# Performance work log

Hardware: AMD Instinct MI355X
Metric: run time of the kernel (lower is better)

## Reference

```python
import jax, jax.numpy as jnp
import numpy as np

DIM = 1024
HEADS = 16
HEAD_DIM = DIM // HEADS
MLP = 4 * DIM
EPS = 1e-5


def layer_norm(x, g, b):
    mu = jnp.mean(x, axis=-1, keepdims=True)
    var = jnp.var(x, axis=-1, keepdims=True)
    return (x - mu) * jax.lax.rsqrt(var + EPS) * g + b


def rope_cos_sin(n, d):
    inv_freq = 1.0 / (10000.0 ** (jnp.arange(0, d, 2, dtype=jnp.float32) / d))
    t = jnp.arange(n, dtype=jnp.float32)
    freqs = jnp.outer(t, inv_freq)          # [N, d/2]
    emb = jnp.concatenate([freqs, freqs], -1)  # [N, d]
    return jnp.cos(emb), jnp.sin(emb)


def rotate_half(x):
    x1, x2 = x[..., ::2], x[..., 1::2]
    return jnp.concatenate([-x2, x1], axis=-1)


def setup_inputs() -> dict:
    key = jax.random.key(0)
    ks = jax.random.split(key, 16)
    B, N = 2, 2048
    s = lambda fan_in: 1.0 / np.sqrt(fan_in)
    inp = {
        "x": jax.random.normal(ks[0], (B, N, DIM), jnp.float32),
        "t_emb": jax.random.normal(ks[1], (B, DIM), jnp.float32),
        "norm1_g": jnp.ones((DIM,), jnp.float32),
        "norm1_b": jnp.zeros((DIM,), jnp.float32),
        "Wq": jax.random.normal(ks[2], (DIM, DIM), jnp.float32) * s(DIM),
        "Wk": jax.random.normal(ks[3], (DIM, DIM), jnp.float32) * s(DIM),
        "Wv": jax.random.normal(ks[4], (DIM, DIM), jnp.float32) * s(DIM),
        "Wo": jax.random.normal(ks[5], (DIM, DIM), jnp.float32) * s(DIM),
        "norm2_g": jnp.ones((DIM,), jnp.float32),
        "norm2_b": jnp.zeros((DIM,), jnp.float32),
        "W1": jax.random.normal(ks[6], (DIM, MLP), jnp.float32) * s(DIM),
        "W2": jax.random.normal(ks[7], (MLP, DIM), jnp.float32) * s(MLP),
        "ada_W": jax.random.normal(ks[8], (DIM, 6 * DIM), jnp.float32) * s(DIM),
        "ada_b": jnp.zeros((6 * DIM,), jnp.float32),
    }
    return inp


def reference(x, t_emb, norm1_g, norm1_b, Wq, Wk, Wv, Wo,
              norm2_g, norm2_b, W1, W2, ada_W, ada_b):
    B, N, C = x.shape
    H, D = HEADS, HEAD_DIM
    scale = D ** -0.5

    mod = jax.nn.silu(t_emb) @ ada_W + ada_b          # [B, 6C]
    (shift_msa, scale_msa, gate_msa,
     shift_mlp, scale_mlp, gate_mlp) = jnp.split(mod, 6, axis=-1)

    xn = layer_norm(x, norm1_g, norm1_b) * (1 + scale_msa[:, None, :]) + shift_msa[:, None, :]

    q = (xn @ Wq).reshape(B, N, H, D).transpose(0, 2, 1, 3)  # [B,H,N,D]
    k = (xn @ Wk).reshape(B, N, H, D).transpose(0, 2, 1, 3)
    v = (xn @ Wv).reshape(B, N, H, D).transpose(0, 2, 1, 3)

    cos, sin = rope_cos_sin(N, D)                     # [N, D]
    q = q * cos + rotate_half(q) * sin
    k = k * cos + rotate_half(k) * sin

    attn = jnp.einsum('bhnd,bhmd->bhnm', q, k) * scale  # explicit O(N^2) scores
    attn = jax.nn.softmax(attn, axis=-1)
    out = jnp.einsum('bhnm,bhmd->bhnd', attn, v)

    out = out.transpose(0, 2, 1, 3).reshape(B, N, C) @ Wo
    x = x + gate_msa[:, None, :] * out

    xn = layer_norm(x, norm2_g, norm2_b) * (1 + scale_mlp[:, None, :]) + shift_mlp[:, None, :]
    mlp = jax.nn.gelu(xn @ W1, approximate=False) @ W2
    x = x + gate_mlp[:, None, :] * mlp
    return x
```

## Files before the change

### kernel.cpp

```cpp
#include <hip/hip_runtime.h>
#include <math.h>

#define BB    2
#define NN    2048
#define CDIM  1024
#define HEADS 16
#define HDIM  64
#define MLPD  4096
#define MODC  6144
#define EPSV  1e-5f
#define LOG2E 1.4426950408889634f
#define MSPLIT 16

typedef __attribute__((ext_vector_type(8))) short s8v;
typedef __attribute__((ext_vector_type(4))) float f4v;

__device__ inline unsigned short f2bf(float f) {
  union { float f; unsigned u; } v; v.f = f;
  unsigned r = v.u + 0x7FFFu + ((v.u >> 16) & 1u);
  return (unsigned short)(r >> 16);
}
__device__ inline float bf2f(unsigned short h) {
  union { unsigned u; float f; } v; v.u = ((unsigned)h) << 16;
  return v.f;
}

template<int CTRL>
__device__ __forceinline__ float dpp_max_step(float v) {
  int iv = __float_as_int(v);
  int sh = __builtin_amdgcn_update_dpp(iv, iv, CTRL, 0xF, 0xF, false);
  return fmaxf(v, __int_as_float(sh));
}
__device__ __forceinline__ float max16(float v) {
  v = dpp_max_step<0xB1>(v);
  v = dpp_max_step<0x4E>(v);
  v = dpp_max_step<0x124>(v);
  v = dpp_max_step<0x128>(v);
  return v;
}

__global__ __launch_bounds__(256) void mod_part(
    const float* __restrict__ t_emb, const float* __restrict__ ada_W,
    float* __restrict__ part) {
  int j = blockIdx.x * 256 + threadIdx.x;
  int b = blockIdx.y, ks = blockIdx.z;
  __shared__ float st[64];
  if (threadIdx.x < 64) {
    float v = t_emb[b * CDIM + ks * 64 + threadIdx.x];
    st[threadIdx.x] = v / (1.0f + expf(-v));
  }
  __syncthreads();
  float acc = 0.f;
  const float* wp = ada_W + (size_t)(ks * 64) * MODC + j;
  #pragma unroll 8
  for (int i = 0; i < 64; ++i) acc += st[i] * wp[(size_t)i * MODC];
  part[((size_t)ks * BB + b) * MODC + j] = acc;
}

__global__ __launch_bounds__(256) void mod_reduce(
    const float* __restrict__ part, const float* __restrict__ ada_b,
    float* __restrict__ mod) {
  int idx = blockIdx.x * 256 + threadIdx.x;
  int b = idx / MODC, j = idx % MODC;
  float a = ada_b[j];
  #pragma unroll
  for (int s = 0; s < MSPLIT; ++s) a += part[((size_t)s * BB + b) * MODC + j];
  mod[(size_t)b * MODC + j] = a;
}

__device__ inline float wave_sum64(float v) {
  for (int o = 32; o > 0; o >>= 1) v += __shfl_down(v, o, 64);
  return v;
}

__global__ __launch_bounds__(256) void ln_mod_bf16(
    const float* __restrict__ x, const float* __restrict__ g,
    const float* __restrict__ bta, const float* __restrict__ mod,
    int shift_off, int scale_off, unsigned short* __restrict__ out) {
  int r = blockIdx.x;
  int b = r / NN;
  int t = threadIdx.x;
  const float* xr = x + (size_t)r * CDIM;
  float4 xv = ((const float4*)xr)[t];
  float s  = xv.x + xv.y + xv.z + xv.w;
  float s2 = xv.x*xv.x + xv.y*xv.y + xv.z*xv.z + xv.w*xv.w;
  __shared__ float ws1[4], ws2[4];
  float sw = wave_sum64(s), s2w = wave_sum64(s2);
  int lane = t & 63, wid = t >> 6;
  if (lane == 0) { ws1[wid] = sw; ws2[wid] = s2w; }
  __syncthreads();
  float mu  = (ws1[0] + ws1[1] + ws1[2] + ws1[3]) * (1.0f / CDIM);
  float var = (ws2[0] + ws2[1] + ws2[2] + ws2[3]) * (1.0f / CDIM) - mu * mu;
  float rstd = rsqrtf(var + EPSV);
  const float* mods = mod + (size_t)b * MODC;
  float4 gv = ((const float4*)g)[t];
  float4 bv = ((const float4*)bta)[t];
  float4 sc = ((const float4*)(mods + scale_off))[t];
  float4 sh = ((const float4*)(mods + shift_off))[t];
  ushort4 ov;
  ov.x = f2bf(((xv.x - mu) * rstd * gv.x + bv.x) * (1.0f + sc.x) + sh.x);
  ov.y = f2bf(((xv.y - mu) * rstd * gv.y + bv.y) * (1.0f + sc.y) + sh.y);
  ov.z = f2bf(((xv.z - mu) * rstd * gv.z + bv.z) * (1.0f + sc.z) + sh.z);
  ov.w = f2bf(((xv.w - mu) * rstd * gv.w + bv.w) * (1.0f + sc.w) + sh.w);
  ((ushort4*)(out + (size_t)r * CDIM))[t] = ov;
}

__global__ __launch_bounds__(256) void wcast_all(
    const float* __restrict__ Wq, const float* __restrict__ Wk,
    const float* __restrict__ Wv, const float* __restrict__ Wo,
    const float* __restrict__ W1, const float* __restrict__ W2,
    unsigned short* __restrict__ Wqkvt, unsigned short* __restrict__ Wot,
    unsigned short* __restrict__ W1t, unsigned short* __restrict__ W2t) {
  int bid = blockIdx.x;
  const float* W; unsigned short* Wt; int K, N, t;
  if (bid < 4096) {
    int m = bid >> 10;
    t = bid & 1023;
    K = CDIM; N = CDIM;
    W  = (m == 0) ? Wq : (m == 1) ? Wk : (m == 2) ? Wv : Wo;
    Wt = (m == 3) ? Wot : (Wqkvt + (size_t)m * CDIM * CDIM);
  } else if (bid < 8192) {
    t = bid - 4096; K = CDIM; N = MLPD; W = W1; Wt = W1t;
  } else {
    t = bid - 8192; K = MLPD; N = CDIM; W = W2; Wt = W2t;
  }
  int ntiles = N >> 5;
  int n0 = (t % ntiles) * 32, k0 = (t / ntiles) * 32;
  __shared__ float tile[32][33];
  int tx = threadIdx.x & 31, ty = threadIdx.x >> 5;
  #pragma unroll
  for (int p = 0; p < 4; ++p)
    tile[ty + p * 8][tx] = W[(size_t)(k0 + ty + p * 8) * N + n0 + tx];
  __syncthreads();
  #pragma unroll
  for (int p = 0; p < 4; ++p)
    Wt[(size_t)(n0 + ty + p * 8) * K + k0 + tx] = f2bf(tile[tx][ty + p * 8]);
}

__global__ __launch_bounds__(1024) void mfma_gemm_256(
    const unsigned short* __restrict__ A,
    const unsigned short* __restrict__ Bt,
    int M, int N, int K,
    unsigned short* __restrict__ Ob, unsigned short* __restrict__ Ob2,
    unsigned short* __restrict__ Ob3, int mode) {
  __shared__ unsigned short SH[2 * 32768];
  int tid = threadIdx.x;
  int wave = tid >> 6, lane = tid & 63;
  int quad = lane >> 4, l15 = lane & 15;
  int m0 = blockIdx.y * 256, n0 = blockIdx.x * 256;
  int wr = wave >> 2, wc = wave & 3;

  f4v acc[4][4] = {};

  int srow = lane >> 3;
  int ksrc = ((lane & 7) ^ (lane >> 3)) << 3;
  const int nt = K >> 6;

  #define STAGE_256(T, BUF)                                                    \
    {                                                                          \
      int k0_ = (T) << 6;                                                      \
      unsigned short* ab = SH + (BUF) * 32768 + wave * 1024;                   \
      _Pragma("unroll")                                                        \
      for (int s = 0; s < 2; ++s) {                                            \
        const unsigned short* ga =                                             \
            A + (size_t)(m0 + 16 * wave + 8 * s + srow) * K + k0_ + ksrc;      \
        __builtin_amdgcn_global_load_lds(                                      \
            (const __attribute__((address_space(1))) unsigned int*)(const void*)ga, \
            (__attribute__((address_space(3))) unsigned int*)(void*)(ab + s * 512), \
            16, 0, 0);                                                         \
        const unsigned short* gb =                                             \
            Bt + (size_t)(n0 + 16 * wave + 8 * s + srow) * K + k0_ + ksrc;     \
        __builtin_amdgcn_global_load_lds(                                      \
            (const __attribute__((address_space(1))) unsigned int*)(const void*)gb, \
            (__attribute__((address_space(3))) unsigned int*)(void*)(ab + 16384 + s * 512), \
            16, 0, 0);                                                         \
      }                                                                        \
    }

  STAGE_256(0, 0);
  asm volatile("s_waitcnt vmcnt(0)" ::: "memory");
  __syncthreads();

  int buf = 0;
  for (int t = 0; t < nt; ++t) {
    if (t + 1 < nt) STAGE_256(t + 1, buf ^ 1);

    const unsigned short* Ab = SH + buf * 32768;
    const unsigned short* Bb = Ab + 16384;
    #pragma unroll
    for (int ks = 0; ks < 2; ++ks) {
      int kx = (ks * 32 + quad * 8) ^ ((l15 & 7) << 3);
      s8v af[4], bf[4];
      #pragma unroll
      for (int i = 0; i < 4; ++i)
        af[i] = *(const s8v*)(Ab + (wr * 64 + i * 16 + l15) * 64 + kx);
      #pragma unroll
      for (int j = 0; j < 4; ++j)
        bf[j] = *(const s8v*)(Bb + (wc * 64 + j * 16 + l15) * 64 + kx);
      #pragma unroll
      for (int i = 0; i < 4; ++i)
        #pragma unroll
        for (int j = 0; j < 4; ++j)
          acc[i][j] = __builtin_amdgcn_mfma_f32_16x16x32_bf16(
              af[i], bf[j], acc[i][j], 0, 0, 0);
    }

    if (t + 1 < nt) {
      asm volatile("s_waitcnt vmcnt(0)" ::: "memory");
      __syncthreads();
      buf ^= 1;
    }
  }
  #undef STAGE_256

  #pragma unroll
  for (int i = 0; i < 4; ++i) {
    int rbase = m0 + wr * 64 + i * 16 + quad * 4;
    #pragma unroll
    for (int j = 0; j < 4; ++j) {
      int c = n0 + wc * 64 + j * 16 + l15;
      #pragma unroll
      for (int rg = 0; rg < 4; ++rg) {
        int r = rbase + rg;
        float v = acc[i][j][rg];
        if (mode == 0) {
          unsigned short* dst = (c < 1024) ? Ob : ((c < 2048) ? Ob2 : Ob3);
          dst[(size_t)r * 1024 + (c & 1023)] = f2bf(v);
        } else {
          v = 0.5f * v * (1.0f + erff(v * 0.70710678118f));
          Ob[(size_t)r * N + c] = f2bf(v);
        }
      }
    }
  }
}

__global__ __launch_bounds__(1024) void mfma_gemm_res(
    const unsigned short* __restrict__ A,
    const unsigned short* __restrict__ Bt,
    int M, int N, int K,
    float* __restrict__ O0,
    const float* __restrict__ res, const float* __restrict__ mod,
    int gate_off) {
  __shared__ unsigned short SH[3 * 16384];
  int tid = threadIdx.x;
  int wave = tid >> 6, lane = tid & 63;
  int quad = lane >> 4, l15 = lane & 15;
  int m0 = blockIdx.y * 128, n0 = blockIdx.x * 128;
  int pos = wave & 7;
  int om = pos >> 1, on = pos & 1;
  int ks = wave >> 3;

  f4v acc[2][4] = {};

  int srow = lane >> 3;
  int ksrc = ((lane & 7) ^ (lane >> 3)) << 3;
  const int nt = K >> 6;

  #define STAGE_RES(T, BUF)                                                    \
    {                                                                          \
      int k0_ = (T) << 6;                                                      \
      unsigned short* dsta = SH + (BUF) * 16384 + wave * 512;                  \
      const unsigned short* ga =                                               \
          A + (size_t)(m0 + 8 * wave + srow) * K + k0_ + ksrc;                 \
      __builtin_amdgcn_global_load_lds(                                        \
          (const __attribute__((address_space(1))) unsigned int*)(const void*)ga, \
          (__attribute__((address_space(3))) unsigned int*)(void*)dsta,        \
          16, 0, 0);                                                           \
      const unsigned short* gb =                                               \
          Bt + (size_t)(n0 + 8 * wave + srow) * K + k0_ + ksrc;                \
      __builtin_amdgcn_global_load_lds(                                        \
          (const __attribute__((address_space(1))) unsigned int*)(const void*)gb, \
          (__attribute__((address_space(3))) unsigned int*)(void*)(dsta + 8192), \
          16, 0, 0);                                                           \
    }

  STAGE_RES(0, 0);
  STAGE_RES(1, 1);
  asm volatile("s_waitcnt vmcnt(2)" ::: "memory");
  __syncthreads();

  int kx = (ks * 32 + quad * 8) ^ ((l15 & 7) << 3);

  int rbuf = 0, sbuf = 2;
  for (int t = 0; t < nt; ++t) {
    if (t + 2 < nt) STAGE_RES(t + 2, sbuf);

    const unsigned short* base = SH + rbuf * 16384;
    s8v af[2], bf[4];
    #pragma unroll
    for (int i = 0; i < 2; ++i)
      af[i] = *(const s8v*)(base + (om * 32 + i * 16 + l15) * 64 + kx);
    #pragma unroll
    for (int j = 0; j < 4; ++j)
      bf[j] = *(const s8v*)(base + 8192 + (on * 64 + j * 16 + l15) * 64 + kx);
    #pragma unroll
    for (int i = 0; i < 2; ++i)
      #pragma unroll
      for (int j = 0; j < 4; ++j)
        acc[i][j] = __builtin_amdgcn_mfma_f32_16x16x32_bf16(
            af[i], bf[j], acc[i][j], 0, 0, 0);

    if (t + 2 < nt) {
      asm volatile("s_waitcnt vmcnt(2)" ::: "memory");
    } else if (t + 1 < nt) {
      asm volatile("s_waitcnt vmcnt(0)" ::: "memory");
    }
    __syncthreads();
    rbuf = (rbuf == 2) ? 0 : rbuf + 1;
    sbuf = (sbuf == 2) ? 0 : sbuf + 1;
  }
  #undef STAGE_RES

  float* red = (float*)SH;
  if (wave >= 8) {
    int rb = (wave - 8) * 2304 + lane * 36;
    #pragma unroll
    for (int i = 0; i < 2; ++i)
      #pragma unroll
      for (int j = 0; j < 4; ++j)
        *(f4v*)(red + rb + (i * 4 + j) * 4) = acc[i][j];
  }
  __syncthreads();
  if (wave < 8) {
    int rb = wave * 2304 + lane * 36;
    #pragma unroll
    for (int i = 0; i < 2; ++i)
      #pragma unroll
      for (int j = 0; j < 4; ++j)
        acc[i][j] += *(const f4v*)(red + rb + (i * 4 + j) * 4);
    #pragma unroll
    for (int i = 0; i < 2; ++i) {
      int rbase = m0 + om * 32 + i * 16 + quad * 4;
      #pragma unroll
      for (int j = 0; j < 4; ++j) {
        int c = n0 + on * 64 + j * 16 + l15;
        #pragma unroll
        for (int rg = 0; rg < 4; ++rg) {
          int r = rbase + rg;
          int bb2 = r >> 11;
          O0[(size_t)r * N + c] =
              res[(size_t)r * N + c] + mod[bb2 * MODC + gate_off + c] * acc[i][j][rg];
        }
      }
    }
  }
}

__global__ __launch_bounds__(256) void rope_qk(
    unsigned short* __restrict__ qb, const unsigned short* __restrict__ kb,
    unsigned short* __restrict__ kpack, float qscale) {
  int r = blockIdx.x;
  int b = r / NN, n = r % NN;
  int t = threadIdx.x;
  int isK = blockIdx.y;
  const unsigned short* src = isK ? kb : qb;
  float scale = isK ? 1.0f : qscale;
  __shared__ float row[CDIM];
  __shared__ float csv[32], snv[32];
  if (t < 32) {
    float invf = powf(10000.0f, -(float)t / 32.0f);
    float sn, cs;
    sincosf((float)n * invf, &sn, &cs);
    csv[t] = cs * scale; snv[t] = sn * scale;
  }
  const unsigned short* qr = src + (size_t)r * CDIM;
  ushort4 xv = ((const ushort4*)qr)[t];
  row[t * 4 + 0] = bf2f(xv.x);
  row[t * 4 + 1] = bf2f(xv.y);
  row[t * 4 + 2] = bf2f(xv.z);
  row[t * 4 + 3] = bf2f(xv.w);
  __syncthreads();
  unsigned short o[4];
  int c0 = t * 4;
  #pragma unroll
  for (int q4 = 0; q4 < 4; ++q4) {
    int c = c0 + q4;
    int h = c >> 6, d = c & 63;
    int i = d & 31;
    float rh = (d < 32) ? -row[h * 64 + 2 * d + 1] : row[h * 64 + 2 * (d - 32)];
    o[q4] = f2bf(row[c] * csv[i] + rh * snv[i]);
  }
  if (!isK) {
    ((ushort4*)(qb + (size_t)r * CDIM))[t] = make_ushort4(o[0], o[1], o[2], o[3]);
  } else {
    int h = c0 >> 6, d0 = c0 & 63;
    int half = d0 >> 5, quad = (d0 >> 3) & 3, j0 = d0 & 7;
    int bh = b * HEADS + h;
    int tt = n >> 6, kt = (n >> 4) & 3, l15 = n & 15;
    int lane = quad * 16 + l15;
    size_t off = ((((size_t)bh * 32 + tt) * 8 + kt * 2 + half) * 64 + lane) * 8 + j0;
    unsigned int lo = (unsigned)o[0] | ((unsigned)o[1] << 16);
    unsigned int hi = (unsigned)o[2] | ((unsigned)o[3] << 16);
    *(uint2*)(kpack + off) = make_uint2(lo, hi);
  }
}

__global__ __launch_bounds__(256) void vtrans_pack(
    const unsigned short* __restrict__ vrow, unsigned short* __restrict__ vpack) {
  int t = blockIdx.x;
  int bh = blockIdx.y;
  int b = bh >> 4, h = bh & 15;
  __shared__ unsigned short L[64 * 72];
  int tid = threadIdx.x;
  #pragma unroll
  for (int p = 0; p < 2; ++p) {
    int c = tid + p * 256;
    int key = c >> 3, dc = (c & 7) * 8;
    *(s8v*)(L + key * 72 + dc) =
        *(const s8v*)(vrow + (size_t)(b * NN + t * 64 + key) * CDIM + h * HDIM + dc);
  }
  __syncthreads();
  #pragma unroll
  for (int p = 0; p < 2; ++p) {
    int o = tid + p * 256;
    int f = o >> 6, lane = o & 63;
    int dt = f >> 1, half = f & 1, quad = lane >> 4, l15 = lane & 15;
    int d = dt * 16 + l15;
    unsigned short tmp[8];
    #pragma unroll
    for (int j = 0; j < 8; ++j) {
      int key = (j & 3) * 16 + half * 8 + quad * 2 + (j >> 2);
      tmp[j] = L[key * 72 + d];
    }
    *(s8v*)(vpack + ((((size_t)bh * 32 + t) * 8 + f) * 64 + lane) * 8) = *(s8v*)tmp;
  }
}

__global__ __launch_bounds__(512) void fattn_pack(
    const unsigned short* __restrict__ qb,
    const unsigned short* __restrict__ kpack,
    const unsigned short* __restrict__ vpack,
    unsigned short* __restrict__ ob) {
  int bid = blockIdx.x;
  int qt = bid >> 5, bh = bid & 31;
  int b = bh >> 4, h = bh & 15;
  int tid = threadIdx.x;
  int wave = tid >> 6, lane = tid & 63;
  int quad = lane >> 4, l15 = lane & 15;

  __shared__ unsigned short smem[3 * 8192 + 8 * 2304];
  unsigned short* Pw = smem + 3 * 8192 + wave * 2304;

  int n0 = qt * 256;
  s8v qf[2][2];
  #pragma unroll
  for (int fq = 0; fq < 2; ++fq) {
    int qrow = n0 + wave * 32 + fq * 16 + l15;
    const unsigned short* qp = qb + (size_t)(b * NN + qrow) * CDIM + h * HDIM;
    qf[fq][0] = *(const s8v*)(qp + quad * 8);
    qf[fq][1] = *(const s8v*)(qp + 32 + quad * 8);
  }

  f4v acc[2][4] = {};
  float m_i[2][4], l_i[2][4];
  #pragma unroll
  for (int fq = 0; fq < 2; ++fq)
    #pragma unroll
    for (int r = 0; r < 4; ++r) { m_i[fq][r] = -1e30f; l_i[fq][r] = 0.f; }

  const unsigned short* ksrc = kpack + (size_t)bh * 131072 + wave * 512 + lane * 8;
  const unsigned short* vsrc = vpack + (size_t)bh * 131072 + wave * 512 + lane * 8;

  #define STAGE_ATT(T, BUF)                                                    \
    {                                                                          \
      __builtin_amdgcn_global_load_lds(                                        \
          (const __attribute__((address_space(1))) unsigned int*)(const void*)(ksrc + (size_t)(T) * 4096), \
          (__attribute__((address_space(3))) unsigned int*)(void*)(smem + (BUF) * 8192 + wave * 512), \
          16, 0, 0);                                                           \
      __builtin_amdgcn_global_load_lds(                                        \
          (const __attribute__((address_space(1))) unsigned int*)(const void*)(vsrc + (size_t)(T) * 4096), \
          (__attribute__((address_space(3))) unsigned int*)(void*)(smem + (BUF) * 8192 + 4096 + wave * 512), \
          16, 0, 0);                                                           \
    }

  const int NT = NN / 64;
  STAGE_ATT(0, 0);
  STAGE_ATT(1, 1);
  asm volatile("s_waitcnt vmcnt(2)" ::: "memory");
  __syncthreads();

  int rbuf = 0, sbuf = 2;
  for (int t = 0; t < NT; ++t) {
    if (t + 2 < NT) STAGE_ATT(t + 2, sbuf);

    const unsigned short* kb_ = smem + rbuf * 8192 + lane * 8;
    f4v s4[2][4];
    {
      s8v kf[8];
      #pragma unroll
      for (int f = 0; f < 8; ++f) kf[f] = *(const s8v*)(kb_ + f * 512);
      #pragma unroll
      for (int fq = 0; fq < 2; ++fq)
        #pragma unroll
        for (int kt = 0; kt < 4; ++kt) {
          f4v z = {};
          z = __builtin_amdgcn_mfma_f32_16x16x32_bf16(qf[fq][0], kf[kt * 2], z, 0, 0, 0);
          z = __builtin_amdgcn_mfma_f32_16x16x32_bf16(qf[fq][1], kf[kt * 2 + 1], z, 0, 0, 0);
          s4[fq][kt] = z;
        }
    }

    #pragma unroll
    for (int fq = 0; fq < 2; ++fq)
      #pragma unroll
      for (int r = 0; r < 4; ++r) {
        float mv = fmaxf(fmaxf(s4[fq][0][r], s4[fq][1][r]),
                         fmaxf(s4[fq][2][r], s4[fq][3][r]));
        mv = max16(mv);
        if (!__all(mv - m_i[fq][r] <= 8.0f)) {
          float mnew = fmaxf(m_i[fq][r], mv);
          float alpha = __builtin_amdgcn_exp2f(m_i[fq][r] - mnew);
          m_i[fq][r] = mnew;
          l_i[fq][r] *= alpha;
          acc[fq][0][r] *= alpha; acc[fq][1][r] *= alpha;
          acc[fq][2][r] *= alpha; acc[fq][3][r] *= alpha;
        }
        float ls = 0.f;
        #pragma unroll
        for (int kt = 0; kt < 4; ++kt) {
          float p = __builtin_amdgcn_exp2f(s4[fq][kt][r] - m_i[fq][r]);
          s4[fq][kt][r] = p;
          ls += p;
        }
        l_i[fq][r] += ls;
      }

    #pragma unroll
    for (int fq = 0; fq < 2; ++fq)
      #pragma unroll
      for (int r = 0; r < 4; ++r) {
        unsigned int lo = (__float_as_uint(s4[fq][0][r]) >> 16) |
                          (__float_as_uint(s4[fq][1][r]) & 0xffff0000u);
        unsigned int hi = (__float_as_uint(s4[fq][2][r]) >> 16) |
                          (__float_as_uint(s4[fq][3][r]) & 0xffff0000u);
        *(uint2*)(Pw + (fq * 16 + quad * 4 + r) * 72 + l15 * 4) = make_uint2(lo, hi);
      }

    {
      const unsigned short* vb_ = smem + rbuf * 8192 + 4096 + lane * 8;
      s8v vf[8];
      #pragma unroll
      for (int f = 0; f < 8; ++f) vf[f] = *(const s8v*)(vb_ + f * 512);
      #pragma unroll
      for (int fq = 0; fq < 2; ++fq) {
        s8v pf0 = *(const s8v*)(Pw + (fq * 16 + l15) * 72 + quad * 8);
        s8v pf1 = *(const s8v*)(Pw + (fq * 16 + l15) * 72 + 32 + quad * 8);
        #pragma unroll
        for (int dt = 0; dt < 4; ++dt) {
          acc[fq][dt] = __builtin_amdgcn_mfma_f32_16x16x32_bf16(pf0, vf[dt * 2], acc[fq][dt], 0, 0, 0);
          acc[fq][dt] = __builtin_amdgcn_mfma_f32_16x16x32_bf16(pf1, vf[dt * 2 + 1], acc[fq][dt], 0, 0, 0);
        }
      }
    }

    if (t + 2 < NT) {
      asm volatile("s_waitcnt vmcnt(2)" ::: "memory");
    } else if (t + 1 < NT) {
      asm volatile("s_waitcnt vmcnt(0)" ::: "memory");
    }
    __syncthreads();
    rbuf = (rbuf == 2) ? 0 : rbuf + 1;
    sbuf = (sbuf == 2) ? 0 : sbuf + 1;
  }
  #undef STAGE_ATT

  #pragma unroll
  for (int fq = 0; fq < 2; ++fq)
    #pragma unroll
    for (int r = 0; r < 4; ++r) {
      float l = l_i[fq][r];
      #pragma unroll
      for (int msk = 1; msk < 16; msk <<= 1)
        l += __shfl_xor(l, msk, 64);
      float inv = 1.0f / l;
      size_t row = (size_t)(b * NN + n0 + wave * 32 + fq * 16 + quad * 4 + r);
      unsigned short* op = ob + row * CDIM + h * HDIM;
      #pragma unroll
      for (int dt = 0; dt < 4; ++dt)
        op[dt * 16 + l15] = f2bf(acc[fq][dt][r] * inv);
    }
}

extern "C" void kernel_launch(void* const* d_in, const int* in_sizes, int n_in,
                              void* d_out, int out_size, void* d_ws, size_t ws_size,
                              hipStream_t stream) {
  const float* x    = (const float*)d_in[0];
  const float* temb = (const float*)d_in[1];
  const float* n1g  = (const float*)d_in[2];
  const float* n1b  = (const float*)d_in[3];
  const float* Wq   = (const float*)d_in[4];
  const float* Wk   = (const float*)d_in[5];
  const float* Wv   = (const float*)d_in[6];
  const float* Wo   = (const float*)d_in[7];
  const float* n2g  = (const float*)d_in[8];
  const float* n2b  = (const float*)d_in[9];
  const float* W1   = (const float*)d_in[10];
  const float* W2   = (const float*)d_in[11];
  const float* adaW = (const float*)d_in[12];
  const float* adab = (const float*)d_in[13];
  float* out = (float*)d_out;

  const size_t TOK = (size_t)BB * NN * CDIM;
  float* wsf = (float*)d_ws;
  float* mod     = wsf;
  float* modpart = wsf + 16384;
  unsigned short* tokb  = (unsigned short*)(wsf + 16384 + MSPLIT * BB * MODC);
  unsigned short* qb    = tokb + TOK;
  unsigned short* kb    = qb + TOK;
  unsigned short* kpack = kb + TOK;
  unsigned short* vpack = kpack + TOK;
  unsigned short* Wqkvt = vpack + TOK;
  unsigned short* Wot   = Wqkvt + 3 * CDIM * CDIM;
  unsigned short* W1t   = Wot + CDIM * CDIM;
  unsigned short* W2t   = W1t + CDIM * MLPD;
  unsigned short* h1b   = W2t + MLPD * CDIM;
  unsigned short* vrow  = h1b;
  float* x1 = (float*)qb;

  const int M = BB * NN;

  mod_part<<<dim3(MODC / 256, BB, MSPLIT), 256, 0, stream>>>(temb, adaW, modpart);
  mod_reduce<<<dim3(BB * MODC / 256), 256, 0, stream>>>(modpart, adab, mod);
  ln_mod_bf16<<<dim3(M), 256, 0, stream>>>(x, n1g, n1b, mod, 0, 1024, tokb);

  wcast_all<<<dim3(12288), 256, 0, stream>>>(
      Wq, Wk, Wv, Wo, W1, W2, Wqkvt, Wot, W1t, W2t);

  mfma_gemm_256<<<dim3(3 * CDIM / 256, M / 256), 1024, 0, stream>>>(
      tokb, Wqkvt, M, 3 * CDIM, CDIM, qb, kb, vrow, 0);

  rope_qk<<<dim3(M, 2), 256, 0, stream>>>(qb, kb, kpack, 0.125f * LOG2E);

  vtrans_pack<<<dim3(NN / 64, BB * HEADS), 256, 0, stream>>>(vrow, vpack);

  fattn_pack<<<dim3((NN / 256) * BB * HEADS), 512, 0, stream>>>(
      qb, kpack, vpack, tokb);

  mfma_gemm_res<<<dim3(CDIM / 128, M / 128), 1024, 0, stream>>>(
      tokb, Wot, M, CDIM, CDIM, x1, x, mod, 2048);

  ln_mod_bf16<<<dim3(M), 256, 0, stream>>>(x1, n2g, n2b, mod, 3072, 4096, tokb);

  mfma_gemm_256<<<dim3(MLPD / 256, M / 256), 1024, 0, stream>>>(
      tokb, W1t, M, MLPD, CDIM, h1b, nullptr, nullptr, 1);

  mfma_gemm_res<<<dim3(CDIM / 128, M / 128), 1024, 0, stream>>>(
      h1b, W2t, M, CDIM, MLPD, out, x1, mod, 5120);
}
```

Baseline: 389.1 us.

## Split-K the W2 down-projection GEMM and combine partials with residual

Replaces the final W2 GEMM (K=4096, 256 blocks of 128x128) with a split-K version that launches twice as many blocks, each covering half of K and writing fp32 partial sums into reused workspace buffers. A new elementwise kernel then sums the two partials, applies the gate and adds the residual. This aims to fill more compute units on a GEMM whose grid is small relative to the device. The cost is an extra round trip of two fp32 M×1024 partial buffers through memory and one more kernel launch.

```diff
diff --git a/kernel.cpp b/kernel.cpp
--- a/kernel.cpp
+++ b/kernel.cpp
@@ -345,6 +345,131 @@
       }
     }
   }
+}
+
+__global__ __launch_bounds__(1024) void mfma_gemm_part(
+    const unsigned short* __restrict__ A,
+    const unsigned short* __restrict__ Bt,
+    int M, int N, int K, int Kblk,
+    float* __restrict__ P0, float* __restrict__ P1) {
+  __shared__ unsigned short SH[36864];
+  int tid = threadIdx.x;
+  int wave = tid >> 6, lane = tid & 63;
+  int quad = lane >> 4, l15 = lane & 15;
+  int m0 = blockIdx.y * 128, n0 = blockIdx.x * 128;
+  int koff = blockIdx.z * Kblk;
+  int pos = wave & 7;
+  int om = pos >> 1, on = pos & 1;
+  int ks = wave >> 3;
+
+  f4v acc[2][4] = {};
+
+  int srow = lane >> 3;
+  int ksrc = ((lane & 7) ^ (lane >> 3)) << 3;
+  const int nt = Kblk >> 6;
+
+  #define STAGE_P(T, BUF)                                                      \
+    {                                                                          \
+      int k0_ = koff + ((T) << 6);                                             \
+      unsigned short* dsta = SH + (BUF) * 16384 + wave * 512;                  \
+      const unsigned short* ga =                                               \
+          A + (size_t)(m0 + 8 * wave + srow) * K + k0_ + ksrc;                 \
+      __builtin_amdgcn_global_load_lds(                                        \
+          (const __attribute__((address_space(1))) unsigned int*)(const void*)ga, \
+          (__attribute__((address_space(3))) unsigned int*)(void*)dsta,        \
+          16, 0, 0);                                                           \
+      const unsigned short* gb =                                               \
+          Bt + (size_t)(n0 + 8 * wave + srow) * K + k0_ + ksrc;                \
+      __builtin_amdgcn_global_load_lds(                                        \
+          (const __attribute__((address_space(1))) unsigned int*)(const void*)gb, \
+          (__attribute__((address_space(3))) unsigned int*)(void*)(dsta + 8192), \
+          16, 0, 0);                                                           \
+    }
+
+  STAGE_P(0, 0);
+  asm volatile("s_waitcnt vmcnt(0)" ::: "memory");
+  __syncthreads();
+
+  int kx = (ks * 32 + quad * 8) ^ ((l15 & 7) << 3);
+
+  int buf = 0;
+  for (int t = 0; t < nt; ++t) {
+    if (t + 1 < nt) STAGE_P(t + 1, buf ^ 1);
+
+    const unsigned short* base = SH + buf * 16384;
+    s8v af[2], bf[4];
+    #pragma unroll
+    for (int i = 0; i < 2; ++i)
+      af[i] = *(const s8v*)(base + (om * 32 + i * 16 + l15) * 64 + kx);
+    #pragma unroll
+    for (int j = 0; j < 4; ++j)
+      bf[j] = *(const s8v*)(base + 8192 + (on * 64 + j * 16 + l15) * 64 + kx);
+    #pragma unroll
+    for (int i = 0; i < 2; ++i)
+      #pragma unroll
+      for (int j = 0; j < 4; ++j)
+        acc[i][j] = __builtin_amdgcn_mfma_f32_16x16x32_bf16(
+            af[i], bf[j], acc[i][j], 0, 0, 0);
+
+    if (t + 1 < nt) {
+      asm volatile("s_waitcnt vmcnt(0)" ::: "memory");
+      __syncthreads();
+      buf ^= 1;
+    }
+  }
+  #undef STAGE_P
+  __syncthreads();
+
+  float* red = (float*)SH;
+  if (wave >= 8) {
+    int rb = (wave - 8) * 2304 + lane * 36;
+    #pragma unroll
+    for (int i = 0; i < 2; ++i)
+      #pragma unroll
+      for (int j = 0; j < 4; ++j)
+        *(f4v*)(red + rb + (i * 4 + j) * 4) = acc[i][j];
+  }
+  __syncthreads();
+  if (wave < 8) {
+    float* P = blockIdx.z ? P1 : P0;
+    int rb = wave * 2304 + lane * 36;
+    #pragma unroll
+    for (int i = 0; i < 2; ++i)
+      #pragma unroll
+      for (int j = 0; j < 4; ++j)
+        acc[i][j] += *(const f4v*)(red + rb + (i * 4 + j) * 4);
+    #pragma unroll
+    for (int i = 0; i < 2; ++i) {
+      int rbase = m0 + om * 32 + i * 16 + quad * 4;
+      #pragma unroll
+      for (int j = 0; j < 4; ++j) {
+        int c = n0 + on * 64 + j * 16 + l15;
+        #pragma unroll
+        for (int rg = 0; rg < 4; ++rg) {
+          int r = rbase + rg;
+          P[(size_t)r * N + c] = acc[i][j][rg];
+        }
+      }
+    }
+  }
+}
+
+__global__ __launch_bounds__(256) void res_combine(
+    const float* __restrict__ P0, const float* __restrict__ P1,
+    const float* __restrict__ res, const float* __restrict__ mod,
+    int gate_off, float* __restrict__ out) {
+  int r = blockIdx.x, t = threadIdx.x;
+  int b = r >> 11;
+  float4 p0 = ((const float4*)(P0 + (size_t)r * CDIM))[t];
+  float4 p1 = ((const float4*)(P1 + (size_t)r * CDIM))[t];
+  float4 rv = ((const float4*)(res + (size_t)r * CDIM))[t];
+  float4 g  = ((const float4*)(mod + (size_t)b * MODC + gate_off))[t];
+  float4 o;
+  o.x = rv.x + g.x * (p0.x + p1.x);
+  o.y = rv.y + g.y * (p0.y + p1.y);
+  o.z = rv.z + g.z * (p0.z + p1.z);
+  o.w = rv.w + g.w * (p0.w + p1.w);
+  ((float4*)(out + (size_t)r * CDIM))[t] = o;
 }
 
 __global__ __launch_bounds__(256) void rope_qk(
@@ -617,6 +742,8 @@
   unsigned short* h1b   = W2t + MLPD * CDIM;
   unsigned short* vrow  = h1b;
   float* x1 = (float*)qb;
+  float* Pz0 = (float*)kpack;
+  float* Pz1 = (float*)Wqkvt;
 
   const int M = BB * NN;
 
@@ -645,6 +772,7 @@
   mfma_gemm_256<<<dim3(MLPD / 256, M / 256), 1024, 0, stream>>>(
       tokb, W1t, M, MLPD, CDIM, h1b, nullptr, nullptr, 1);
 
-  mfma_gemm_res<<<dim3(CDIM / 128, M / 128), 1024, 0, stream>>>(
-      h1b, W2t, M, CDIM, MLPD, out, x1, mod, 5120);
-}
+  mfma_gemm_part<<<dim3(CDIM / 128, M / 128, 2), 1024, 0, stream>>>(
+      h1b, W2t, M, CDIM, MLPD, MLPD / 2, Pz0, Pz1);
+  res_combine<<<dim3(M), 256, 0, stream>>>(Pz0, Pz1, x1, mod, 5120, out);
+}
```

Result: slower. 398.2 us (+2.3%).
